# Optimization experiments

Measured on AMD Instinct MI355X. Metric: run time of the kernel, lower is better.

## Reference

```python
import jax, jax.numpy as jnp
import numpy as np

HEADS = 4
LEAKY_SLOPE = 0.2  # PyG GATConv default negative_slope


def gat_layer(x, src, dst, W, a_src, a_dst, b):
    """One PyG-style GATConv (concat=True). x:[N,F_in], W:[F_in,H*C]."""
    N = x.shape[0]
    h = (x @ W).reshape(N, HEADS, -1)                    # [N,H,C]
    alpha_src = jnp.sum(h * a_src, axis=-1)              # [N,H]
    alpha_dst = jnp.sum(h * a_dst, axis=-1)              # [N,H]
    e = jax.nn.leaky_relu(alpha_src[src] + alpha_dst[dst], LEAKY_SLOPE)  # [E,H]
    # numerically stable softmax over edges grouped by destination node
    emax = jax.ops.segment_max(e, dst, num_segments=N)   # [N,H]
    emax = jnp.where(jnp.isfinite(emax), emax, 0.0)
    ex = jnp.exp(e - emax[dst])                          # [E,H]
    denom = jax.ops.segment_sum(ex, dst, num_segments=N) # [N,H]
    alpha = ex / (denom[dst] + 1e-16)                    # [E,H]
    out = jax.ops.segment_sum(h[src] * alpha[:, :, None], dst, num_segments=N)  # [N,H,C]
    return out.reshape(N, -1) + b


def setup_inputs() -> dict:
    key = jax.random.key(0)
    ks = jax.random.split(key, 10)
    N, E = 100000, 1600000
    IN, HID, OUT = 128, 128, 128
    c1, c2 = HID // HEADS, OUT // HEADS
    x = jax.random.normal(ks[0], (N, IN), jnp.float32)
    edge_index = jax.random.randint(ks[1], (2, E), 0, N, jnp.int32)
    s_in, s_h = 1.0 / np.sqrt(IN), 1.0 / np.sqrt(HID)
    W1 = jax.random.normal(ks[2], (IN, HEADS * c1), jnp.float32) * s_in
    a_src1 = jax.random.normal(ks[3], (HEADS, c1), jnp.float32) * 0.1
    a_dst1 = jax.random.normal(ks[4], (HEADS, c1), jnp.float32) * 0.1
    b1 = jnp.zeros((HEADS * c1,), jnp.float32)
    W2 = jax.random.normal(ks[5], (HID, HEADS * c2), jnp.float32) * s_h
    a_src2 = jax.random.normal(ks[6], (HEADS, c2), jnp.float32) * 0.1
    a_dst2 = jax.random.normal(ks[7], (HEADS, c2), jnp.float32) * 0.1
    b2 = jnp.zeros((HEADS * c2,), jnp.float32)
    return {"x": x, "edge_index": edge_index, "W1": W1, "a_src1": a_src1,
            "a_dst1": a_dst1, "b1": b1, "W2": W2, "a_src2": a_src2,
            "a_dst2": a_dst2, "b2": b2}


def reference(x, edge_index, W1, a_src1, a_dst1, b1, W2, a_src2, a_dst2, b2):
    N = x.shape[0]
    # PyG GATConv default: add self-loops
    loop = jnp.arange(N, dtype=edge_index.dtype)
    src = jnp.concatenate([edge_index[0], loop])
    dst = jnp.concatenate([edge_index[1], loop])
    h = gat_layer(x, src, dst, W1, a_src1, a_dst1, b1)
    h = jax.nn.elu(h)  # ELU between layers
    out = gat_layer(h, src, dst, W2, a_src2, a_dst2, b2)
    per_head = jnp.split(out, HEADS, axis=-1)
    return (out, *per_head)
```

## Files before the change

kernel.cpp:

```cpp
#include <hip/hip_runtime.h>
#include <hip/hip_fp16.h>
#include <cstddef>
#include <cstdint>

#define LEAKY 0.2f
#define CAP   64
#define BKSH  7
#define BKN   128
#define SUBC  8
#define SCAP  512

__device__ __forceinline__ float lrelu(float x) {
    return x > 0.f ? x : LEAKY * x;
}

#define GROWS 64
__global__ __launch_bounds__(256) void gemm128_k(const float* __restrict__ A,
                                                 const float* __restrict__ Wg,
                                                 const float* __restrict__ a_s,
                                                 const float* __restrict__ a_d,
                                                 __half* __restrict__ H,
                                                 float* __restrict__ asrc,
                                                 float* __restrict__ adst, int M)
{
    __shared__ float As[GROWS][129];
    int t  = threadIdx.x;
    int r0 = blockIdx.x * GROWS;

#pragma unroll
    for (int i = 0; i < 8; ++i) {
        int f   = t + i * 256;
        int row = f >> 5;
        int k4  = (f & 31) * 4;
        int gr  = r0 + row;
        if (gr >= M) gr = M - 1;
        float4 v = *(const float4*)(A + (size_t)gr * 128 + k4);
        As[row][k4 + 0] = v.x;
        As[row][k4 + 1] = v.y;
        As[row][k4 + 2] = v.z;
        As[row][k4 + 3] = v.w;
    }
    __syncthreads();

    int row = t & 63;
    int cg  = __builtin_amdgcn_readfirstlane(t >> 6);
    const float* __restrict__ wbase = Wg + cg * 32;

    float acc[32];
#pragma unroll
    for (int j = 0; j < 32; ++j) acc[j] = 0.f;

#pragma unroll 2
    for (int k = 0; k < 128; ++k) {
        float a = As[row][k];
        const float* __restrict__ wr = wbase + k * 128;
#pragma unroll
        for (int j = 0; j < 32; ++j)
            acc[j] += a * wr[j];
    }

    int gr = r0 + row;
    if (gr < M) {
        __half hv[32];
#pragma unroll
        for (int j = 0; j < 32; ++j) hv[j] = __float2half(acc[j]);
        float4* o = (float4*)((char*)H + (size_t)gr * 256 + cg * 64);
#pragma unroll
        for (int j4 = 0; j4 < 4; ++j4)
            o[j4] = ((const float4*)hv)[j4];

        float ps = 0.f, pd = 0.f;
#pragma unroll
        for (int j = 0; j < 32; ++j) {
            ps += acc[j] * a_s[cg * 32 + j];
            pd += acc[j] * a_d[cg * 32 + j];
        }
        asrc[(size_t)gr * 4 + cg] = ps;
        adst[(size_t)gr * 4 + cg] = pd;
    }
}

__global__ __launch_bounds__(256) void gemm_build_k(
    const float* __restrict__ A, const float* __restrict__ Wg,
    const float* __restrict__ a_s, const float* __restrict__ a_d,
    __half* __restrict__ H, float* __restrict__ asrc,
    float* __restrict__ adst, int M,
    const int* __restrict__ srcv, const int* __restrict__ dstv, int E, int EPB,
    int* __restrict__ bcur, uint2* __restrict__ bpair)
{
    __shared__ float As[GROWS][129];
    int t  = threadIdx.x;
    int r0 = blockIdx.x * GROWS;
    int cls = blockIdx.x & (SUBC - 1);

    int ebase = blockIdx.x * EPB;
    int ne = E - ebase;
    if (ne > EPB) ne = EPB;
    int d[4], s[4];
#pragma unroll
    for (int i = 0; i < 4; ++i) {
        int idx = t + i * 256;
        bool ok = idx < ne;
        int e = ebase + idx;
        d[i] = ok ? dstv[ok ? e : 0] : -1;
        s[i] = ok ? srcv[ok ? e : 0] : 0;
    }

#pragma unroll
    for (int i = 0; i < 8; ++i) {
        int f   = t + i * 256;
        int row = f >> 5;
        int k4  = (f & 31) * 4;
        int gr  = r0 + row;
        if (gr >= M) gr = M - 1;
        float4 v = *(const float4*)(A + (size_t)gr * 128 + k4);
        As[row][k4 + 0] = v.x;
        As[row][k4 + 1] = v.y;
        As[row][k4 + 2] = v.z;
        As[row][k4 + 3] = v.w;
    }
    __syncthreads();

    int r[4];
#pragma unroll
    for (int i = 0; i < 4; ++i) {
        int q = (d[i] >> BKSH) * SUBC + cls;
        r[i] = (d[i] >= 0) ? atomicAdd(&bcur[q], 1) : 0;
    }

    int row = t & 63;
    int cg  = __builtin_amdgcn_readfirstlane(t >> 6);
    const float* __restrict__ wbase = Wg + cg * 32;

    float acc[32];
#pragma unroll
    for (int j = 0; j < 32; ++j) acc[j] = 0.f;

#pragma unroll 2
    for (int k = 0; k < 128; ++k) {
        float a = As[row][k];
        const float* __restrict__ wr = wbase + k * 128;
#pragma unroll
        for (int j = 0; j < 32; ++j)
            acc[j] += a * wr[j];
    }

#pragma unroll
    for (int i = 0; i < 4; ++i) {
        if (d[i] >= 0 && r[i] < SCAP) {
            int q = (d[i] >> BKSH) * SUBC + cls;
            bpair[(size_t)q * SCAP + r[i]] =
                make_uint2((unsigned)s[i], (unsigned)d[i]);
        }
    }

    int gr = r0 + row;
    if (gr < M) {
        __half hv[32];
#pragma unroll
        for (int j = 0; j < 32; ++j) hv[j] = __float2half(acc[j]);
        float4* o = (float4*)((char*)H + (size_t)gr * 256 + cg * 64);
#pragma unroll
        for (int j4 = 0; j4 < 4; ++j4)
            o[j4] = ((const float4*)hv)[j4];

        float ps = 0.f, pd = 0.f;
#pragma unroll
        for (int j = 0; j < 32; ++j) {
            ps += acc[j] * a_s[cg * 32 + j];
            pd += acc[j] * a_d[cg * 32 + j];
        }
        asrc[(size_t)gr * 4 + cg] = ps;
        adst[(size_t)gr * 4 + cg] = pd;
    }
}

__global__ __launch_bounds__(256) void bin_scatter_k(
    const int* __restrict__ bcur, const uint2* __restrict__ bpair,
    int* __restrict__ cnt, int* __restrict__ adjp, int N)
{
    __shared__ int cntL[BKN];
    __shared__ int adjL[BKN * CAP];

    int b = blockIdx.x;
    int t = threadIdx.x;
    if (t < BKN) cntL[t] = 0;
    __syncthreads();

#pragma unroll 1
    for (int c = 0; c < SUBC; ++c) {
        int q = b * SUBC + c;
        int m = bcur[q];
        if (m > SCAP) m = SCAP;
        const uint2* __restrict__ bp = bpair + (size_t)q * SCAP;
        for (int i = t; i < m; i += 256) {
            uint2 pr = bp[i];
            int ln = (int)(pr.y & (BKN - 1));
            int r = atomicAdd(&cntL[ln], 1);
            if (r < CAP) adjL[(ln << 6) + r] = (int)pr.x;
        }
    }
    __syncthreads();

    int4* __restrict__ dst4 = (int4*)(adjp + (size_t)b * BKN * CAP);
    const int4* __restrict__ src4 = (const int4*)adjL;
#pragma unroll
    for (int i = 0; i < BKN * CAP / 4 / 256; ++i)
        dst4[t + i * 256] = src4[t + i * 256];
    if (t < BKN) {
        int n = b * BKN + t;
        if (n < N) cnt[n] = cntL[t];
    }
}

__global__ __launch_bounds__(256) void aggregate_k(
    const int* __restrict__ cnt_g, const int* __restrict__ adjp,
    const __half* __restrict__ h, const float* __restrict__ asrc,
    const float* __restrict__ adst, const float* __restrict__ bias,
    float* __restrict__ out, int N, int final_flag)
{
    __shared__ float    s_w[4][CAP][4];
    __shared__ unsigned s_off[4][CAP];

    int wv = __builtin_amdgcn_readfirstlane(threadIdx.x >> 6);
    int l  = threadIdx.x & 63;
    int n  = blockIdx.x * 4 + wv;
    if (n >= N) return;
    int g  = l >> 4;
    int q  = l & 15;
    int hq = q >> 2;

    int cnt = cnt_g[n];
    if (cnt > CAP) cnt = CAP;

    float4 ad4 = ((const float4*)adst)[n];
    float4 as4 = ((const float4*)asrc)[n];
    float e_self = lrelu(((const float*)&as4)[g] + ((const float*)&ad4)[g]);

    const char* __restrict__ hb = (const char*)h;

    if (l < cnt) {
        int s = adjp[(size_t)n * CAP + l];
        s_off[wv][l] = (unsigned)s << 8;
        float4 a4 = ((const float4*)asrc)[s];
        float4 wl;
        wl.x = lrelu(a4.x + ad4.x);
        wl.y = lrelu(a4.y + ad4.y);
        wl.z = lrelu(a4.z + ad4.z);
        wl.w = lrelu(a4.w + ad4.w);
        *(float4*)&s_w[wv][l][0] = wl;
    }
    asm volatile("s_waitcnt lgkmcnt(0)" ::: "memory");
    __builtin_amdgcn_wave_barrier();

    float m = e_self;
    for (int j = q; j < cnt; j += 16)
        m = fmaxf(m, s_w[wv][j][g]);
#pragma unroll
    for (int mk = 8; mk > 0; mk >>= 1)
        m = fmaxf(m, __shfl_xor(m, mk, 64));

    float ws = 0.f;
    for (int j = q; j < cnt; j += 16) {
        float w = __expf(s_w[wv][j][g] - m);
        s_w[wv][j][g] = w;
        ws += w;
    }
#pragma unroll
    for (int mk = 8; mk > 0; mk >>= 1)
        ws += __shfl_xor(ws, mk, 64);
    float wself = __expf(e_self - m);
    float ssum  = ws + wself;

    asm volatile("s_waitcnt lgkmcnt(0)" ::: "memory");
    __builtin_amdgcn_wave_barrier();

    float inv  = 1.f / (ssum + 1e-16f);
    float invh = __shfl(inv,   hq << 4, 64);
    float wsh  = __shfl(wself, hq << 4, 64);

    unsigned qoff    = (unsigned)q * 16u;
    unsigned selfoff = ((unsigned)n << 8) + qoff;
    float acc[8];
    {
        float4 raw = *(const float4*)(hb + selfoff);
        const __half2* hp = (const __half2*)&raw;
        float sw = (g == 0) ? wsh : 0.f;
#pragma unroll
        for (int i = 0; i < 4; ++i) {
            float2 f = __half22float2(hp[i]);
            acc[2 * i]     = sw * f.x;
            acc[2 * i + 1] = sw * f.y;
        }
    }

#pragma unroll 2
    for (int j = 0; j < cnt; j += 4) {
        int e = j + g;
        bool v = e < cnt;
        float w = v ? s_w[wv][e][hq] : 0.f;
        unsigned off = (v ? s_off[wv][e] : ((unsigned)n << 8)) + qoff;
        float4 raw = *(const float4*)(hb + off);
        const __half2* hp = (const __half2*)&raw;
#pragma unroll
        for (int i = 0; i < 4; ++i) {
            float2 f = __half22float2(hp[i]);
            acc[2 * i]     = fmaf(w, f.x, acc[2 * i]);
            acc[2 * i + 1] = fmaf(w, f.y, acc[2 * i + 1]);
        }
    }

#pragma unroll
    for (int i = 0; i < 8; ++i) {
        acc[i] += __shfl_xor(acc[i], 16, 64);
        acc[i] += __shfl_xor(acc[i], 32, 64);
    }

    if (g == 0) {
        float o8[8];
        const float* bq = bias + 8 * q;
#pragma unroll
        for (int i = 0; i < 8; ++i)
            o8[i] = acc[i] * invh + bq[i];
        if (final_flag) {
            float4* o = (float4*)(out + (size_t)n * 128 + 8 * q);
            o[0] = ((const float4*)o8)[0];
            o[1] = ((const float4*)o8)[1];
            int ch = (8 * q) & 31;
            float4* o2 = (float4*)(out + (size_t)N * 128
                          + (size_t)hq * N * 32 + (size_t)n * 32 + ch);
            o2[0] = ((const float4*)o8)[0];
            o2[1] = ((const float4*)o8)[1];
        } else {
#pragma unroll
            for (int i = 0; i < 8; ++i)
                o8[i] = o8[i] > 0.f ? o8[i] : expm1f(o8[i]);
            float4* o = (float4*)(out + (size_t)n * 128 + 8 * q);
            o[0] = ((const float4*)o8)[0];
            o[1] = ((const float4*)o8)[1];
        }
    }
}

extern "C" void kernel_launch(void* const* d_in, const int* in_sizes, int n_in,
                              void* d_out, int out_size, void* d_ws, size_t ws_size,
                              hipStream_t stream)
{
    const float* x   = (const float*)d_in[0];
    const int*   ei  = (const int*)d_in[1];
    const float* W1  = (const float*)d_in[2];
    const float* aS1 = (const float*)d_in[3];
    const float* aD1 = (const float*)d_in[4];
    const float* b1  = (const float*)d_in[5];
    const float* W2  = (const float*)d_in[6];
    const float* aS2 = (const float*)d_in[7];
    const float* aD2 = (const float*)d_in[8];
    const float* b2  = (const float*)d_in[9];
    float* out = (float*)d_out;

    int N = in_sizes[0] / 128;
    int E = in_sizes[1] / 2;
    const int* srcv = ei;
    const int* dstv = ei + E;

    char* p = (char*)d_ws;
    auto alloc = [&](size_t bytes) {
        char* r = p;
        p += (bytes + 255) & ~(size_t)255;
        return r;
    };
    int NBK = (N + BKN - 1) >> BKSH;
    __half* h    = (__half*)alloc((size_t)N * 128 * 2);
    float* x2     = (float*)alloc((size_t)N * 128 * 4);
    float* asrc   = (float*)alloc((size_t)N * 4 * 4);
    float* adst   = (float*)alloc((size_t)N * 4 * 4);
    int*   cnt    = (int*)alloc((size_t)N * 4);
    int*   adjp   = (int*)alloc((size_t)NBK * BKN * CAP * 4);
    int*   bcur   = (int*)alloc((size_t)NBK * SUBC * 4);
    uint2* bpair  = (uint2*)alloc((size_t)NBK * SUBC * SCAP * 8);

    hipMemsetAsync(bcur, 0, (size_t)NBK * SUBC * 4, stream);

    int gemm_grid = (N + GROWS - 1) / GROWS;
    int EPB       = (E + gemm_grid - 1) / gemm_grid;
    int agg_grid  = (N + 3) / 4;

    gemm_build_k<<<gemm_grid, 256, 0, stream>>>(
        x, W1, aS1, aD1, h, asrc, adst, N, srcv, dstv, E, EPB, bcur, bpair);
    bin_scatter_k<<<NBK, 256, 0, stream>>>(bcur, bpair, cnt, adjp, N);
    aggregate_k<<<agg_grid, 256, 0, stream>>>(cnt, adjp, h, asrc, adst, b1, x2, N, 0);

    gemm128_k<<<gemm_grid, 256, 0, stream>>>(x2, W2, aS2, aD2, h, asrc, adst, N);
    aggregate_k<<<agg_grid, 256, 0, stream>>>(cnt, adjp, h, asrc, adst, b2, out, N, 1);
}
```

Before: 503.8 us.

## Bin edges per block via shared-memory histogram into coarse 512-node buckets

Edge binning now builds a per-block histogram over 512-node buckets, does a block-wide prefix scan, and sorts edges locally in shared memory. It then reserves space in each global bucket with a single atomic per bucket instead of one global atomic per edge, and stores each pair packed into 32 bits (src shifted, local dst). The scatter kernel processes one larger bucket per block and writes the adjacency list directly to global memory. This cuts global atomic contention and halves pair traffic, at the cost of extra shared-memory sort work, bounded bucket capacity and a 256-bucket limit that requires N of at most 131072.

```diff
diff --git a/kernel.cpp b/kernel.cpp
--- a/kernel.cpp
+++ b/kernel.cpp
@@ -5,10 +5,9 @@
 
 #define LEAKY 0.2f
 #define CAP   64
-#define BKSH  7
-#define BKN   128
-#define SUBC  8
-#define SCAP  512
+#define BSH   9
+#define BNODES 512
+#define BCAP  12288
 
 __device__ __forceinline__ float lrelu(float x) {
     return x > 0.f ? x : LEAKY * x;
@@ -86,16 +85,21 @@
     __half* __restrict__ H, float* __restrict__ asrc,
     float* __restrict__ adst, int M,
     const int* __restrict__ srcv, const int* __restrict__ dstv, int E, int EPB,
-    int* __restrict__ bcur, uint2* __restrict__ bpair)
+    int NBUK, int* __restrict__ gcur, unsigned* __restrict__ bpair)
 {
     __shared__ float As[GROWS][129];
+    __shared__ unsigned prL[1024];
+    __shared__ unsigned char pbL[1024];
+    __shared__ int hist[256], lstart[256], lcur[256], gbaseL[256];
+    __shared__ int wsum[4];
+
     int t  = threadIdx.x;
     int r0 = blockIdx.x * GROWS;
-    int cls = blockIdx.x & (SUBC - 1);
 
     int ebase = blockIdx.x * EPB;
     int ne = E - ebase;
     if (ne > EPB) ne = EPB;
+    if (ne < 0) ne = 0;
     int d[4], s[4];
 #pragma unroll
     for (int i = 0; i < 4; ++i) {
@@ -119,14 +123,48 @@
         As[row][k4 + 2] = v.z;
         As[row][k4 + 3] = v.w;
     }
-    __syncthreads();
-
-    int r[4];
+    hist[t] = 0;
+    __syncthreads();
+
+#pragma unroll
+    for (int i = 0; i < 4; ++i)
+        if (d[i] >= 0) atomicAdd(&hist[d[i] >> BSH], 1);
+    __syncthreads();
+
+    int lane = t & 63, wvid = t >> 6;
+    int v = (t < NBUK) ? hist[t] : 0;
+    int x = v;
+#pragma unroll
+    for (int off = 1; off < 64; off <<= 1) {
+        int y = __shfl_up(x, off, 64);
+        if (lane >= off) x += y;
+    }
+    if (lane == 63) wsum[wvid] = x;
+    __syncthreads();
+    if (t == 0) {
+        int run = 0;
+#pragma unroll
+        for (int w = 0; w < 4; ++w) { int sc = wsum[w]; wsum[w] = run; run += sc; }
+    }
+    __syncthreads();
+    int excl = (x - v) + wsum[wvid];
+    if (t < NBUK) { lstart[t] = excl; lcur[t] = excl; }
+    __syncthreads();
+
 #pragma unroll
     for (int i = 0; i < 4; ++i) {
-        int q = (d[i] >> BKSH) * SUBC + cls;
-        r[i] = (d[i] >= 0) ? atomicAdd(&bcur[q], 1) : 0;
-    }
+        if (d[i] >= 0) {
+            int b = d[i] >> BSH;
+            int pos = atomicAdd(&lcur[b], 1);
+            prL[pos] = ((unsigned)s[i] << BSH) | (unsigned)(d[i] & (BNODES - 1));
+            pbL[pos] = (unsigned char)b;
+        }
+    }
+    __syncthreads();
+
+    int gb = 0;
+    if (t < NBUK && v > 0)
+        gb = atomicAdd(&gcur[t], v);
 
     int row = t & 63;
     int cg  = __builtin_amdgcn_readfirstlane(t >> 6);
@@ -145,13 +183,12 @@
             acc[j] += a * wr[j];
     }
 
-#pragma unroll
-    for (int i = 0; i < 4; ++i) {
-        if (d[i] >= 0 && r[i] < SCAP) {
-            int q = (d[i] >> BKSH) * SUBC + cls;
-            bpair[(size_t)q * SCAP + r[i]] =
-                make_uint2((unsigned)s[i], (unsigned)d[i]);
-        }
+    if (t < NBUK) gbaseL[t] = gb;
+    __syncthreads();
+    for (int p = t; p < ne; p += 256) {
+        int b = pbL[p];
+        unsigned idx = (unsigned)gbaseL[b] + (unsigned)(p - lstart[b]);
+        if (idx < BCAP) bpair[(size_t)b * BCAP + idx] = prL[p];
     }
 
     int gr = r0 + row;
@@ -176,40 +213,33 @@
 }
 
 __global__ __launch_bounds__(256) void bin_scatter_k(
-    const int* __restrict__ bcur, const uint2* __restrict__ bpair,
+    const int* __restrict__ gcur, const unsigned* __restrict__ bpair,
     int* __restrict__ cnt, int* __restrict__ adjp, int N)
 {
-    __shared__ int cntL[BKN];
-    __shared__ int adjL[BKN * CAP];
-
+    __shared__ int cntL[BNODES];
     int b = blockIdx.x;
     int t = threadIdx.x;
-    if (t < BKN) cntL[t] = 0;
-    __syncthreads();
-
-#pragma unroll 1
-    for (int c = 0; c < SUBC; ++c) {
-        int q = b * SUBC + c;
-        int m = bcur[q];
-        if (m > SCAP) m = SCAP;
-        const uint2* __restrict__ bp = bpair + (size_t)q * SCAP;
-        for (int i = t; i < m; i += 256) {
-            uint2 pr = bp[i];
-            int ln = (int)(pr.y & (BKN - 1));
-            int r = atomicAdd(&cntL[ln], 1);
-            if (r < CAP) adjL[(ln << 6) + r] = (int)pr.x;
-        }
-    }
-    __syncthreads();
-
-    int4* __restrict__ dst4 = (int4*)(adjp + (size_t)b * BKN * CAP);
-    const int4* __restrict__ src4 = (const int4*)adjL;
-#pragma unroll
-    for (int i = 0; i < BKN * CAP / 4 / 256; ++i)
-        dst4[t + i * 256] = src4[t + i * 256];
-    if (t < BKN) {
-        int n = b * BKN + t;
-        if (n < N) cnt[n] = cntL[t];
+    cntL[t] = 0;
+    cntL[t + 256] = 0;
+    __syncthreads();
+
+    int m = gcur[b];
+    if (m > BCAP) m = BCAP;
+    const unsigned* __restrict__ bp = bpair + (size_t)b * BCAP;
+    int nb = b << BSH;
+
+    for (int i = t; i < m; i += 256) {
+        unsigned w = bp[i];
+        int ln  = (int)(w & (BNODES - 1));
+        int src = (int)(w >> BSH);
+        int r = atomicAdd(&cntL[ln], 1);
+        if (r < CAP) adjp[((size_t)(nb + ln) << 6) + r] = src;
+    }
+    __syncthreads();
+
+    for (int i = t; i < BNODES; i += 256) {
+        int n = nb + i;
+        if (n < N) cnt[n] = cntL[i];
     }
 }
 
@@ -297,9 +327,9 @@
 #pragma unroll 2
     for (int j = 0; j < cnt; j += 4) {
         int e = j + g;
-        bool v = e < cnt;
-        float w = v ? s_w[wv][e][hq] : 0.f;
-        unsigned off = (v ? s_off[wv][e] : ((unsigned)n << 8)) + qoff;
+        bool vld = e < cnt;
+        float w = vld ? s_w[wv][e][hq] : 0.f;
+        unsigned off = (vld ? s_off[wv][e] : ((unsigned)n << 8)) + qoff;
         float4 raw = *(const float4*)(hb + off);
         const __half2* hp = (const __half2*)&raw;
 #pragma unroll
@@ -369,25 +399,26 @@
         p += (bytes + 255) & ~(size_t)255;
         return r;
     };
-    int NBK = (N + BKN - 1) >> BKSH;
+    int NBUK = (N + BNODES - 1) >> BSH;
+    int Npad = (N + BNODES - 1) & ~(BNODES - 1);
     __half* h    = (__half*)alloc((size_t)N * 128 * 2);
     float* x2     = (float*)alloc((size_t)N * 128 * 4);
     float* asrc   = (float*)alloc((size_t)N * 4 * 4);
     float* adst   = (float*)alloc((size_t)N * 4 * 4);
     int*   cnt    = (int*)alloc((size_t)N * 4);
-    int*   adjp   = (int*)alloc((size_t)NBK * BKN * CAP * 4);
-    int*   bcur   = (int*)alloc((size_t)NBK * SUBC * 4);
-    uint2* bpair  = (uint2*)alloc((size_t)NBK * SUBC * SCAP * 8);
-
-    hipMemsetAsync(bcur, 0, (size_t)NBK * SUBC * 4, stream);
+    int*   adjp   = (int*)alloc((size_t)Npad * CAP * 4);
+    int*   gcur   = (int*)alloc((size_t)NBUK * 4);
+    unsigned* bpair = (unsigned*)alloc((size_t)NBUK * BCAP * 4);
+
+    hipMemsetAsync(gcur, 0, (size_t)NBUK * 4, stream);
 
     int gemm_grid = (N + GROWS - 1) / GROWS;
     int EPB       = (E + gemm_grid - 1) / gemm_grid;
     int agg_grid  = (N + 3) / 4;
 
     gemm_build_k<<<gemm_grid, 256, 0, stream>>>(
-        x, W1, aS1, aD1, h, asrc, adst, N, srcv, dstv, E, EPB, bcur, bpair);
-    bin_scatter_k<<<NBK, 256, 0, stream>>>(bcur, bpair, cnt, adjp, N);
+        x, W1, aS1, aD1, h, asrc, adst, N, srcv, dstv, E, EPB, NBUK, gcur, bpair);
+    bin_scatter_k<<<NBUK, 256, 0, stream>>>(gcur, bpair, cnt, adjp, N);
     aggregate_k<<<agg_grid, 256, 0, stream>>>(cnt, adjp, h, asrc, adst, b1, x2, N, 0);
 
     gemm128_k<<<gemm_grid, 256, 0, stream>>>(x2, W2, aS2, aD2, h, asrc, adst, N);
```

Result: slower. 533.1 us (+5.8%).

## Use split-fp16 MFMA for both GAT projection GEMMs

Applied to the files above, without the earlier changes.

Replaces the scalar FP32 FMA GEMM in both projection kernels with MFMA 16x16x32 f16 instructions. To keep near-FP32 accuracy, each operand is split into high and low fp16 parts, and three MFMAs per tile (hi*hi, lo*hi, hi*lo) are accumulated. A small kernel pre-transposes and splits W1/W2 each call. The attention dot products are now reduced with cross-lane shuffles, and the output tile is staged through LDS for coalesced half stores. This adds a launch and extra LDS traffic in exchange for matrix-core throughput.

```diff
diff --git a/kernel.cpp b/kernel.cpp
--- a/kernel.cpp
+++ b/kernel.cpp
@@ -10,23 +10,40 @@
 #define SUBC  8
 #define SCAP  512
 
+typedef _Float16 f16x8 __attribute__((ext_vector_type(8)));
+typedef _Float16 f16x4 __attribute__((ext_vector_type(4)));
+typedef float    f32x4 __attribute__((ext_vector_type(4)));
+
 __device__ __forceinline__ float lrelu(float x) {
     return x > 0.f ? x : LEAKY * x;
 }
 
+__global__ __launch_bounds__(256) void wsplit_k(
+    const float* __restrict__ W1, const float* __restrict__ W2,
+    _Float16* __restrict__ WtHi1, _Float16* __restrict__ WtLo1,
+    _Float16* __restrict__ WtHi2, _Float16* __restrict__ WtLo2)
+{
+    int idx = blockIdx.x * 256 + threadIdx.x;
+    const float* W = (idx < 16384) ? W1 : W2;
+    _Float16* Hh = (idx < 16384) ? WtHi1 : WtHi2;
+    _Float16* Hl = (idx < 16384) ? WtLo1 : WtLo2;
+    int i = idx & 16383;
+    int j = i >> 7, k = i & 127;
+    float v = W[k * 128 + j];
+    _Float16 hi = (_Float16)v;
+    _Float16 lo = (_Float16)(v - (float)hi);
+    Hh[j * 128 + k] = hi;
+    Hl[j * 128 + k] = lo;
+}
+
 #define GROWS 64
-__global__ __launch_bounds__(256) void gemm128_k(const float* __restrict__ A,
-                                                 const float* __restrict__ Wg,
-                                                 const float* __restrict__ a_s,
-                                                 const float* __restrict__ a_d,
-                                                 __half* __restrict__ H,
-                                                 float* __restrict__ asrc,
-                                                 float* __restrict__ adst, int M)
-{
-    __shared__ float As[GROWS][129];
-    int t  = threadIdx.x;
-    int r0 = blockIdx.x * GROWS;
-
+#define ASTR  136
+
+__device__ __forceinline__ void stage_tile(const float* __restrict__ A, int M,
+                                           int r0, int t,
+                                           _Float16* __restrict__ Ahi,
+                                           _Float16* __restrict__ Alo)
+{
 #pragma unroll
     for (int i = 0; i < 8; ++i) {
         int f   = t + i * 256;
@@ -35,62 +52,134 @@
         int gr  = r0 + row;
         if (gr >= M) gr = M - 1;
         float4 v = *(const float4*)(A + (size_t)gr * 128 + k4);
-        As[row][k4 + 0] = v.x;
-        As[row][k4 + 1] = v.y;
-        As[row][k4 + 2] = v.z;
-        As[row][k4 + 3] = v.w;
-    }
+        _Float16 h0 = (_Float16)v.x, h1 = (_Float16)v.y;
+        _Float16 h2 = (_Float16)v.z, h3 = (_Float16)v.w;
+        f16x4 hv = {h0, h1, h2, h3};
+        f16x4 lv = {(_Float16)(v.x - (float)h0), (_Float16)(v.y - (float)h1),
+                    (_Float16)(v.z - (float)h2), (_Float16)(v.w - (float)h3)};
+        *(f16x4*)&Ahi[row * ASTR + k4] = hv;
+        *(f16x4*)&Alo[row * ASTR + k4] = lv;
+    }
+}
+
+__device__ __forceinline__ void mfma_core(const _Float16* __restrict__ Ahi,
+                                          const _Float16* __restrict__ Alo,
+                                          const _Float16* __restrict__ WtHi,
+                                          const _Float16* __restrict__ WtLo,
+                                          int w, int lr, int lq,
+                                          f32x4 (&acc)[4][2])
+{
+    const _Float16* bH = WtHi + (size_t)(w * 32 + lr) * 128 + lq * 8;
+    const _Float16* bL = WtLo + (size_t)(w * 32 + lr) * 128 + lq * 8;
+#pragma unroll
+    for (int ks = 0; ks < 4; ++ks) {
+        f16x8 b0h = *(const f16x8*)(bH + ks * 32);
+        f16x8 b1h = *(const f16x8*)(bH + 16 * 128 + ks * 32);
+        f16x8 b0l = *(const f16x8*)(bL + ks * 32);
+        f16x8 b1l = *(const f16x8*)(bL + 16 * 128 + ks * 32);
+#pragma unroll
+        for (int it = 0; it < 4; ++it) {
+            const int ao = (it * 16 + lr) * ASTR + ks * 32 + lq * 8;
+            f16x8 ah = *(const f16x8*)&Ahi[ao];
+            f16x8 al = *(const f16x8*)&Alo[ao];
+            acc[it][0] = __builtin_amdgcn_mfma_f32_16x16x32_f16(ah, b0h, acc[it][0], 0, 0, 0);
+            acc[it][0] = __builtin_amdgcn_mfma_f32_16x16x32_f16(al, b0h, acc[it][0], 0, 0, 0);
+            acc[it][0] = __builtin_amdgcn_mfma_f32_16x16x32_f16(ah, b0l, acc[it][0], 0, 0, 0);
+            acc[it][1] = __builtin_amdgcn_mfma_f32_16x16x32_f16(ah, b1h, acc[it][1], 0, 0, 0);
+            acc[it][1] = __builtin_amdgcn_mfma_f32_16x16x32_f16(al, b1h, acc[it][1], 0, 0, 0);
+            acc[it][1] = __builtin_amdgcn_mfma_f32_16x16x32_f16(ah, b1l, acc[it][1], 0, 0, 0);
+        }
+    }
+}
+
+__device__ __forceinline__ void gemm_epilogue(
+    f32x4 (&acc)[4][2], const float* __restrict__ a_s,
+    const float* __restrict__ a_d, __half* __restrict__ H,
+    float* __restrict__ asrc, float* __restrict__ adst, int M,
+    int r0, int t, int w, int lr, int lq, _Float16* __restrict__ Hl)
+{
+    const float* aSw = a_s + w * 32;
+    const float* aDw = a_d + w * 32;
+    float as0 = aSw[lr], as1 = aSw[16 + lr];
+    float ad0 = aDw[lr], ad1 = aDw[16 + lr];
+#pragma unroll
+    for (int it = 0; it < 4; ++it) {
+#pragma unroll
+        for (int rr = 0; rr < 4; ++rr) {
+            float ps = acc[it][0][rr] * as0 + acc[it][1][rr] * as1;
+            float pd = acc[it][0][rr] * ad0 + acc[it][1][rr] * ad1;
+#pragma unroll
+            for (int mk = 8; mk > 0; mk >>= 1) {
+                ps += __shfl_xor(ps, mk, 64);
+                pd += __shfl_xor(pd, mk, 64);
+            }
+            int gr = r0 + it * 16 + lq * 4 + rr;
+            if (lr == 0 && gr < M) {
+                asrc[(size_t)gr * 4 + w] = ps;
+                adst[(size_t)gr * 4 + w] = pd;
+            }
+        }
+    }
+
+    __syncthreads();
+#pragma unroll
+    for (int it = 0; it < 4; ++it)
+#pragma unroll
+        for (int jt = 0; jt < 2; ++jt)
+#pragma unroll
+            for (int rr = 0; rr < 4; ++rr)
+                Hl[(it * 16 + lq * 4 + rr) * ASTR + w * 32 + jt * 16 + lr] =
+                    (_Float16)acc[it][jt][rr];
     __syncthreads();
 
     int row = t & 63;
-    int cg  = __builtin_amdgcn_readfirstlane(t >> 6);
-    const float* __restrict__ wbase = Wg + cg * 32;
-
-    float acc[32];
-#pragma unroll
-    for (int j = 0; j < 32; ++j) acc[j] = 0.f;
-
-#pragma unroll 2
-    for (int k = 0; k < 128; ++k) {
-        float a = As[row][k];
-        const float* __restrict__ wr = wbase + k * 128;
-#pragma unroll
-        for (int j = 0; j < 32; ++j)
-            acc[j] += a * wr[j];
-    }
-
-    int gr = r0 + row;
+    int cg  = t >> 6;
+    int gr  = r0 + row;
     if (gr < M) {
-        __half hv[32];
-#pragma unroll
-        for (int j = 0; j < 32; ++j) hv[j] = __float2half(acc[j]);
         float4* o = (float4*)((char*)H + (size_t)gr * 256 + cg * 64);
 #pragma unroll
         for (int j4 = 0; j4 < 4; ++j4)
-            o[j4] = ((const float4*)hv)[j4];
-
-        float ps = 0.f, pd = 0.f;
-#pragma unroll
-        for (int j = 0; j < 32; ++j) {
-            ps += acc[j] * a_s[cg * 32 + j];
-            pd += acc[j] * a_d[cg * 32 + j];
-        }
-        asrc[(size_t)gr * 4 + cg] = ps;
-        adst[(size_t)gr * 4 + cg] = pd;
-    }
+            o[j4] = *(float4*)&Hl[row * ASTR + cg * 32 + j4 * 8];
+    }
+}
+
+__global__ __launch_bounds__(256) void gemm128_k(
+    const float* __restrict__ A, const _Float16* __restrict__ WtHi,
+    const _Float16* __restrict__ WtLo, const float* __restrict__ a_s,
+    const float* __restrict__ a_d, __half* __restrict__ H,
+    float* __restrict__ asrc, float* __restrict__ adst, int M)
+{
+    __shared__ _Float16 Ahi[GROWS * ASTR];
+    __shared__ _Float16 Alo[GROWS * ASTR];
+    int t  = threadIdx.x;
+    int r0 = blockIdx.x * GROWS;
+    stage_tile(A, M, r0, t, Ahi, Alo);
+    __syncthreads();
+
+    int w  = __builtin_amdgcn_readfirstlane(t >> 6);
+    int l  = t & 63, lr = l & 15, lq = l >> 4;
+    f32x4 acc[4][2];
+#pragma unroll
+    for (int it = 0; it < 4; ++it) {
+        acc[it][0] = (f32x4){0.f, 0.f, 0.f, 0.f};
+        acc[it][1] = (f32x4){0.f, 0.f, 0.f, 0.f};
+    }
+    mfma_core(Ahi, Alo, WtHi, WtLo, w, lr, lq, acc);
+    gemm_epilogue(acc, a_s, a_d, H, asrc, adst, M, r0, t, w, lr, lq, Ahi);
 }
 
 __global__ __launch_bounds__(256) void gemm_build_k(
-    const float* __restrict__ A, const float* __restrict__ Wg,
-    const float* __restrict__ a_s, const float* __restrict__ a_d,
-    __half* __restrict__ H, float* __restrict__ asrc,
-    float* __restrict__ adst, int M,
+    const float* __restrict__ A, const _Float16* __restrict__ WtHi,
+    const _Float16* __restrict__ WtLo, const float* __restrict__ a_s,
+    const float* __restrict__ a_d, __half* __restrict__ H,
+    float* __restrict__ asrc, float* __restrict__ adst, int M,
     const int* __restrict__ srcv, const int* __restrict__ dstv, int E, int EPB,
     int* __restrict__ bcur, uint2* __restrict__ bpair)
 {
-    __shared__ float As[GROWS][129];
-    int t  = threadIdx.x;
-    int r0 = blockIdx.x * GROWS;
+    __shared__ _Float16 Ahi[GROWS * ASTR];
+    __shared__ _Float16 Alo[GROWS * ASTR];
+    int t   = threadIdx.x;
+    int r0  = blockIdx.x * GROWS;
     int cls = blockIdx.x & (SUBC - 1);
 
     int ebase = blockIdx.x * EPB;
@@ -106,19 +195,7 @@
         s[i] = ok ? srcv[ok ? e : 0] : 0;
     }
 
-#pragma unroll
-    for (int i = 0; i < 8; ++i) {
-        int f   = t + i * 256;
-        int row = f >> 5;
-        int k4  = (f & 31) * 4;
-        int gr  = r0 + row;
-        if (gr >= M) gr = M - 1;
-        float4 v = *(const float4*)(A + (size_t)gr * 128 + k4);
-        As[row][k4 + 0] = v.x;
-        As[row][k4 + 1] = v.y;
-        As[row][k4 + 2] = v.z;
-        As[row][k4 + 3] = v.w;
-    }
+    stage_tile(A, M, r0, t, Ahi, Alo);
     __syncthreads();
 
     int r[4];
@@ -128,22 +205,15 @@
         r[i] = (d[i] >= 0) ? atomicAdd(&bcur[q], 1) : 0;
     }
 
-    int row = t & 63;
-    int cg  = __builtin_amdgcn_readfirstlane(t >> 6);
-    const float* __restrict__ wbase = Wg + cg * 32;
-
-    float acc[32];
-#pragma unroll
-    for (int j = 0; j < 32; ++j) acc[j] = 0.f;
-
-#pragma unroll 2
-    for (int k = 0; k < 128; ++k) {
-        float a = As[row][k];
-        const float* __restrict__ wr = wbase + k * 128;
-#pragma unroll
-        for (int j = 0; j < 32; ++j)
-            acc[j] += a * wr[j];
-    }
+    int w  = __builtin_amdgcn_readfirstlane(t >> 6);
+    int l  = t & 63, lr = l & 15, lq = l >> 4;
+    f32x4 acc[4][2];
+#pragma unroll
+    for (int it = 0; it < 4; ++it) {
+        acc[it][0] = (f32x4){0.f, 0.f, 0.f, 0.f};
+        acc[it][1] = (f32x4){0.f, 0.f, 0.f, 0.f};
+    }
+    mfma_core(Ahi, Alo, WtHi, WtLo, w, lr, lq, acc);
 
 #pragma unroll
     for (int i = 0; i < 4; ++i) {
@@ -154,25 +224,7 @@
         }
     }
 
-    int gr = r0 + row;
-    if (gr < M) {
-        __half hv[32];
-#pragma unroll
-        for (int j = 0; j < 32; ++j) hv[j] = __float2half(acc[j]);
-        float4* o = (float4*)((char*)H + (size_t)gr * 256 + cg * 64);
-#pragma unroll
-        for (int j4 = 0; j4 < 4; ++j4)
-            o[j4] = ((const float4*)hv)[j4];
-
-        float ps = 0.f, pd = 0.f;
-#pragma unroll
-        for (int j = 0; j < 32; ++j) {
-            ps += acc[j] * a_s[cg * 32 + j];
-            pd += acc[j] * a_d[cg * 32 + j];
-        }
-        asrc[(size_t)gr * 4 + cg] = ps;
-        adst[(size_t)gr * 4 + cg] = pd;
-    }
+    gemm_epilogue(acc, a_s, a_d, H, asrc, adst, M, r0, t, w, lr, lq, Ahi);
 }
 
 __global__ __launch_bounds__(256) void bin_scatter_k(
@@ -297,9 +349,9 @@
 #pragma unroll 2
     for (int j = 0; j < cnt; j += 4) {
         int e = j + g;
-        bool v = e < cnt;
-        float w = v ? s_w[wv][e][hq] : 0.f;
-        unsigned off = (v ? s_off[wv][e] : ((unsigned)n << 8)) + qoff;
+        bool vld = e < cnt;
+        float w = vld ? s_w[wv][e][hq] : 0.f;
+        unsigned off = (vld ? s_off[wv][e] : ((unsigned)n << 8)) + qoff;
         float4 raw = *(const float4*)(hb + off);
         const __half2* hp = (const __half2*)&raw;
 #pragma unroll
@@ -378,18 +430,23 @@
     int*   adjp   = (int*)alloc((size_t)NBK * BKN * CAP * 4);
     int*   bcur   = (int*)alloc((size_t)NBK * SUBC * 4);
     uint2* bpair  = (uint2*)alloc((size_t)NBK * SUBC * SCAP * 8);
+    _Float16* WtHi1 = (_Float16*)alloc(16384 * 2);
+    _Float16* WtLo1 = (_Float16*)alloc(16384 * 2);
+    _Float16* WtHi2 = (_Float16*)alloc(16384 * 2);
+    _Float16* WtLo2 = (_Float16*)alloc(16384 * 2);
 
     hipMemsetAsync(bcur, 0, (size_t)NBK * SUBC * 4, stream);
+    wsplit_k<<<128, 256, 0, stream>>>(W1, W2, WtHi1, WtLo1, WtHi2, WtLo2);
 
     int gemm_grid = (N + GROWS - 1) / GROWS;
     int EPB       = (E + gemm_grid - 1) / gemm_grid;
     int agg_grid  = (N + 3) / 4;
 
     gemm_build_k<<<gemm_grid, 256, 0, stream>>>(
-        x, W1, aS1, aD1, h, asrc, adst, N, srcv, dstv, E, EPB, bcur, bpair);
+        x, WtHi1, WtLo1, aS1, aD1, h, asrc, adst, N, srcv, dstv, E, EPB, bcur, bpair);
     bin_scatter_k<<<NBK, 256, 0, stream>>>(bcur, bpair, cnt, adjp, N);
     aggregate_k<<<agg_grid, 256, 0, stream>>>(cnt, adjp, h, asrc, adst, b1, x2, N, 0);
 
-    gemm128_k<<<gemm_grid, 256, 0, stream>>>(x2, W2, aS2, aD2, h, asrc, adst, N);
+    gemm128_k<<<gemm_grid, 256, 0, stream>>>(x2, WtHi2, WtLo2, aS2, aD2, h, asrc, adst, N);
     aggregate_k<<<agg_grid, 256, 0, stream>>>(cnt, adjp, h, asrc, adst, b2, out, N, 1);
 }
```

Result: faster. 475.0 us (-5.7%).
